# Kernel tuning notes

Hardware: AMD Instinct MI355X
Metric: run time of the kernel (lower is better)

## Reference

```python
import jax, jax.numpy as jnp
import numpy as np

N_NODES = 100000
N_EDGES = 800000
IN_DIM = 128
HID = 128
N_CLASSES = 4


def setup_inputs() -> dict:
    key = jax.random.key(0)
    ks = jax.random.split(key, 8)
    x = jax.random.normal(ks[0], (N_NODES, IN_DIM), dtype=jnp.float32)
    edge_index = jax.random.randint(ks[1], (2, N_EDGES), 0, N_NODES, dtype=jnp.int32)
    s0 = 1.0 / np.sqrt(IN_DIM)
    s1 = 1.0 / np.sqrt(HID)
    W0 = jax.random.uniform(ks[2], (HID, IN_DIM), minval=-s0, maxval=s0, dtype=jnp.float32)
    b0 = jax.random.uniform(ks[3], (HID,), minval=-s0, maxval=s0, dtype=jnp.float32)
    W1 = jax.random.uniform(ks[4], (HID, HID), minval=-s1, maxval=s1, dtype=jnp.float32)
    b1 = jax.random.uniform(ks[5], (HID,), minval=-s1, maxval=s1, dtype=jnp.float32)
    Wc = jax.random.uniform(ks[6], (N_CLASSES, HID), minval=-s1, maxval=s1, dtype=jnp.float32)
    bc = jax.random.uniform(ks[7], (N_CLASSES,), minval=-s1, maxval=s1, dtype=jnp.float32)
    return {"x": x, "edge_index": edge_index, "W0": W0, "b0": b0,
            "W1": W1, "b1": b1, "Wc": Wc, "bc": bc}


def reference(x, edge_index, W0, b0, W1, b1, Wc, bc):
    row, col = edge_index[0], edge_index[1]
    n = x.shape[0]
    # layer 0: Linear + ReLU (dropout is identity in eval)
    h = jax.nn.relu(x @ W0.T + b0)                                  # [N, HID]
    # scatter-add neighbor aggregation with degree normalization
    agg = jax.ops.segment_sum(h[col], row, num_segments=n)          # [N, HID]
    deg = jax.ops.segment_sum(jnp.ones_like(row, dtype=h.dtype), row, num_segments=n)
    agg = agg / jnp.clip(deg, 1.0)[:, None]
    h = h + agg                                                     # residual add
    # final conv + ReLU + classifier
    h = jax.nn.relu(h @ W1.T + b1)
    logits = h @ Wc.T + bc                                          # [N, N_CLASSES]
    return logits
```

## Files before the change

kernel.cpp:

```cpp
#include <hip/hip_runtime.h>

#define IN_DIM 128
#define HID    128
#define NCLS   4

typedef __attribute__((ext_vector_type(8))) short bf16x8;
typedef __attribute__((ext_vector_type(4))) float f32x4;

__device__ inline ushort f2bf(float x) {
    uint u = __builtin_bit_cast(uint, x);
    u += 0x7FFFu + ((u >> 16) & 1u);
    return (ushort)(u >> 16);
}
__device__ inline float bf2f(ushort h) {
    uint u = ((uint)h) << 16;
    return __builtin_bit_cast(float, u);
}

__device__ inline void gload_lds16(const void* g, void* l) {
    __builtin_amdgcn_global_load_lds((const __attribute__((address_space(1))) void*)g,
                                     (__attribute__((address_space(3))) void*)l, 16, 0, 0);
}

__global__ __launch_bounds__(256) void cast_w(const float* __restrict__ W0,
                                              const float* __restrict__ W1,
                                              ushort* __restrict__ w0h, ushort* __restrict__ w0l,
                                              ushort* __restrict__ w1h, ushort* __restrict__ w1l)
{
    int i = blockIdx.x * 256 + threadIdx.x;
    float v = (i < 16384) ? W0[i] : W1[i - 16384];
    ushort h = f2bf(v);
    ushort l = f2bf(v - bf2f(h));
    if (i < 16384) { w0h[i] = h; w0l[i] = l; }
    else           { w1h[i - 16384] = h; w1l[i - 16384] = l; }
}


__global__ __launch_bounds__(256) void gnn_lin0_mfma(const float* __restrict__ X,
                                                     const ushort* __restrict__ Whi,
                                                     const ushort* __restrict__ Wlo,
                                                     const float* __restrict__ Bv,
                                                     ushort* __restrict__ Hhi,
                                                     ushort* __restrict__ Hlo, int M)
{
    __shared__ uint4 lds4[2048];
    char* lds = (char*)lds4;

    const int tid = threadIdx.x;
    const int bm  = blockIdx.x * 64;

    {
        const int row  = tid >> 2;
        const int seg  = tid & 3;
        const int grow = min(bm + row, M - 1);
        const float4* src = (const float4*)((const char*)X + (size_t)grow * 512 + seg * 128);
        float4 v[8];
        #pragma unroll
        for (int j = 0; j < 8; ++j) v[j] = src[j];

        #pragma unroll
        for (int j = 0; j < 4; ++j) {
            uint hw[4], lw[4];
            #pragma unroll
            for (int q = 0; q < 2; ++q) {
                const float4 f = v[j * 2 + q];
                ushort h0 = f2bf(f.x), h1 = f2bf(f.y), h2 = f2bf(f.z), h3 = f2bf(f.w);
                ushort l0 = f2bf(f.x - bf2f(h0)), l1 = f2bf(f.y - bf2f(h1));
                ushort l2 = f2bf(f.z - bf2f(h2)), l3 = f2bf(f.w - bf2f(h3));
                hw[q * 2]     = (uint)h0 | ((uint)h1 << 16);
                hw[q * 2 + 1] = (uint)h2 | ((uint)h3 << 16);
                lw[q * 2]     = (uint)l0 | ((uint)l1 << 16);
                lw[q * 2 + 1] = (uint)l2 | ((uint)l3 << 16);
            }
            int unit = (seg * 4 + j) ^ (row & 7);
            int off  = row * 256 + unit * 16;
            *(uint4*)(lds + off)         = make_uint4(hw[0], hw[1], hw[2], hw[3]);
            *(uint4*)(lds + 16384 + off) = make_uint4(lw[0], lw[1], lw[2], lw[3]);
        }
    }
    __syncthreads();

    const int wid = tid >> 6, lane = tid & 63;
    const int wr = wid >> 1, wc = wid & 1;
    const int colbase = wc * 64;
    const int lr = lane & 15, lk = lane >> 4;

    f32x4 acc[4][2];
    #pragma unroll
    for (int nt = 0; nt < 4; ++nt)
        #pragma unroll
        for (int rt = 0; rt < 2; ++rt) acc[nt][rt] = (f32x4){0.f, 0.f, 0.f, 0.f};

    #pragma unroll
    for (int kt = 0; kt < 4; ++kt) {
        const int ko = kt * 32 + lk * 8;
        bf16x8 xh[2], xl[2];
        #pragma unroll
        for (int rt = 0; rt < 2; ++rt) {
            int lrow = wr * 32 + rt * 16 + lr;
            int unit = (kt * 4 + lk) ^ (lrow & 7);
            int off  = lrow * 256 + unit * 16;
            xh[rt] = *(const bf16x8*)(lds + off);
            xl[rt] = *(const bf16x8*)(lds + 16384 + off);
        }
        #pragma unroll
        for (int nt = 0; nt < 4; ++nt) {
            size_t bo = (size_t)(colbase + nt * 16 + lr) * 128 + ko;
            bf16x8 wh = *(const bf16x8*)(Whi + bo);
            bf16x8 wl = *(const bf16x8*)(Wlo + bo);
            #pragma unroll
            for (int rt = 0; rt < 2; ++rt) {
                acc[nt][rt] = __builtin_amdgcn_mfma_f32_16x16x32_bf16(wh, xh[rt], acc[nt][rt], 0, 0, 0);
                acc[nt][rt] = __builtin_amdgcn_mfma_f32_16x16x32_bf16(wh, xl[rt], acc[nt][rt], 0, 0, 0);
                acc[nt][rt] = __builtin_amdgcn_mfma_f32_16x16x32_bf16(wl, xh[rt], acc[nt][rt], 0, 0, 0);
            }
        }
    }

    #pragma unroll
    for (int nt = 0; nt < 4; ++nt) {
        const int col0 = colbase + nt * 16 + lk * 4;
        const float4 bv4 = *(const float4*)(Bv + col0);
        const float bvv[4] = {bv4.x, bv4.y, bv4.z, bv4.w};
        #pragma unroll
        for (int rt = 0; rt < 2; ++rt) {
            int row = bm + wr * 32 + rt * 16 + lr;
            float o0 = fmaxf(acc[nt][rt][0] + bvv[0], 0.f);
            float o1 = fmaxf(acc[nt][rt][1] + bvv[1], 0.f);
            float o2 = fmaxf(acc[nt][rt][2] + bvv[2], 0.f);
            float o3 = fmaxf(acc[nt][rt][3] + bvv[3], 0.f);
            ushort4 h4, l4;
            h4.x = f2bf(o0); l4.x = f2bf(o0 - bf2f(h4.x));
            h4.y = f2bf(o1); l4.y = f2bf(o1 - bf2f(h4.y));
            h4.z = f2bf(o2); l4.z = f2bf(o2 - bf2f(h4.z));
            h4.w = f2bf(o3); l4.w = f2bf(o3 - bf2f(h4.w));
            size_t oo = (size_t)row * 128 + col0;
            *(ushort4*)(Hhi + oo) = h4;
            *(ushort4*)(Hlo + oo) = l4;
        }
    }
}

__global__ __launch_bounds__(256) void gnn_lin1_mfma(const ushort* __restrict__ Ahi,
                                                     const ushort* __restrict__ Alo,
                                                     const ushort* __restrict__ Whi,
                                                     const ushort* __restrict__ Wlo,
                                                     const float* __restrict__ Bv,
                                                     const float* __restrict__ Wc,
                                                     const float* __restrict__ bc,
                                                     float* __restrict__ Out, int M)
{
    __shared__ uint4 lds4[2048];
    __shared__ float red[2][64][4];
    char* lds = (char*)lds4;

    const int tid = threadIdx.x;
    const int wid = tid >> 6, lane = tid & 63;
    const int bm  = blockIdx.x * 64;

    #pragma unroll
    for (int i = 0; i < 8; ++i) {
        int o = wid * 8192 + i * 1024 + lane * 16;
        const ushort* plane = (o < 16384) ? Ahi : Alo;
        int po   = o & 16383;
        int row  = po >> 8;
        int unit = (po >> 4) & 15;
        const char* src = (const char*)plane + (size_t)(bm + row) * 256
                        + ((unit ^ (row & 7)) << 4);
        gload_lds16(src, lds + wid * 8192 + i * 1024);
    }
    __syncthreads();

    const int wr = wid >> 1, wc = wid & 1;
    const int colbase = wc * 64;
    const int lr = lane & 15, lk = lane >> 4;

    f32x4 acc[4][2];
    #pragma unroll
    for (int nt = 0; nt < 4; ++nt)
        #pragma unroll
        for (int rt = 0; rt < 2; ++rt) acc[nt][rt] = (f32x4){0.f, 0.f, 0.f, 0.f};

    #pragma unroll
    for (int kt = 0; kt < 4; ++kt) {
        const int ko = kt * 32 + lk * 8;
        bf16x8 xh[2], xl[2];
        #pragma unroll
        for (int rt = 0; rt < 2; ++rt) {
            int lrow = wr * 32 + rt * 16 + lr;
            int unit = (kt * 4 + lk) ^ (lrow & 7);
            int off  = lrow * 256 + unit * 16;
            xh[rt] = *(const bf16x8*)(lds + off);
            xl[rt] = *(const bf16x8*)(lds + 16384 + off);
        }
        #pragma unroll
        for (int nt = 0; nt < 4; ++nt) {
            size_t bo = (size_t)(colbase + nt * 16 + lr) * 128 + ko;
            bf16x8 wh = *(const bf16x8*)(Whi + bo);
            bf16x8 wl = *(const bf16x8*)(Wlo + bo);
            #pragma unroll
            for (int rt = 0; rt < 2; ++rt) {
                acc[nt][rt] = __builtin_amdgcn_mfma_f32_16x16x32_bf16(wh, xh[rt], acc[nt][rt], 0, 0, 0);
                acc[nt][rt] = __builtin_amdgcn_mfma_f32_16x16x32_bf16(wh, xl[rt], acc[nt][rt], 0, 0, 0);
                acc[nt][rt] = __builtin_amdgcn_mfma_f32_16x16x32_bf16(wl, xh[rt], acc[nt][rt], 0, 0, 0);
            }
        }
    }

    float p[2][4] = {{0.f, 0.f, 0.f, 0.f}, {0.f, 0.f, 0.f, 0.f}};
    #pragma unroll
    for (int nt = 0; nt < 4; ++nt) {
        const int col0 = colbase + nt * 16 + lk * 4;
        const float4 bv4 = *(const float4*)(Bv + col0);
        const float bvv[4] = {bv4.x, bv4.y, bv4.z, bv4.w};
        float4 wcr[4];
        #pragma unroll
        for (int c = 0; c < 4; ++c) wcr[c] = *(const float4*)(Wc + c * HID + col0);
        #pragma unroll
        for (int rt = 0; rt < 2; ++rt) {
            float h2v[4];
            #pragma unroll
            for (int r = 0; r < 4; ++r) h2v[r] = fmaxf(acc[nt][rt][r] + bvv[r], 0.f);
            #pragma unroll
            for (int c = 0; c < 4; ++c) {
                const float* w = (const float*)&wcr[c];
                p[rt][c] = fmaf(h2v[0], w[0], p[rt][c]);
                p[rt][c] = fmaf(h2v[1], w[1], p[rt][c]);
                p[rt][c] = fmaf(h2v[2], w[2], p[rt][c]);
                p[rt][c] = fmaf(h2v[3], w[3], p[rt][c]);
            }
        }
    }
    #pragma unroll
    for (int off = 16; off < 64; off <<= 1)
        #pragma unroll
        for (int rt = 0; rt < 2; ++rt)
            #pragma unroll
            for (int c = 0; c < 4; ++c)
                p[rt][c] += __shfl_xor(p[rt][c], off);

    if (lk == 0) {
        #pragma unroll
        for (int rt = 0; rt < 2; ++rt) {
            f32x4 v = {p[rt][0], p[rt][1], p[rt][2], p[rt][3]};
            *(f32x4*)&red[wc][wr * 32 + rt * 16 + lr][0] = v;
        }
    }
    __syncthreads();

    const int row_local = tid >> 2, cls = tid & 3;
    int row = blockIdx.x * 64 + row_local;
    if (row < M) {
        float s = bc[cls] + red[0][row_local][cls] + red[1][row_local][cls];
        Out[(size_t)row * 4 + cls] = s;
    }
}

__global__ __launch_bounds__(256) void count_deg(const int* __restrict__ rows,
                                                 int* __restrict__ deg, int E)
{
    int e = blockIdx.x * 256 + threadIdx.x;
    if (e < E) atomicAdd(&deg[rows[e]], 1);
}

__global__ __launch_bounds__(256) void scan_blocks(const int* __restrict__ deg,
                                                   int* __restrict__ off,
                                                   int* __restrict__ bsum, int M)
{
    __shared__ int sh[256];
    int i = blockIdx.x * 256 + threadIdx.x;
    int v = (i < M) ? deg[i] : 0;
    sh[threadIdx.x] = v;
    __syncthreads();
    #pragma unroll
    for (int d = 1; d < 256; d <<= 1) {
        int t = (threadIdx.x >= d) ? sh[threadIdx.x - d] : 0;
        __syncthreads();
        sh[threadIdx.x] += t;
        __syncthreads();
    }
    if (i < M) off[i] = sh[threadIdx.x] - v;
    if (threadIdx.x == 255) bsum[blockIdx.x] = sh[255];
}

__global__ __launch_bounds__(512) void scan_bsum(int* __restrict__ bsum, int NB)
{
    __shared__ int sh[512];
    int v = (threadIdx.x < NB) ? bsum[threadIdx.x] : 0;
    sh[threadIdx.x] = v;
    __syncthreads();
    #pragma unroll
    for (int d = 1; d < 512; d <<= 1) {
        int t = (threadIdx.x >= d) ? sh[threadIdx.x - d] : 0;
        __syncthreads();
        sh[threadIdx.x] += t;
        __syncthreads();
    }
    if (threadIdx.x < NB) bsum[threadIdx.x] = sh[threadIdx.x] - v;
}

__global__ __launch_bounds__(256) void add_off(int* __restrict__ off,
                                               const int* __restrict__ bsum,
                                               int* __restrict__ pos, int M)
{
    int i = blockIdx.x * 256 + threadIdx.x;
    if (i < M) {
        int o = off[i] + bsum[i >> 8];
        off[i] = o;
        pos[i] = o;
    }
}

__global__ __launch_bounds__(256) void fill_csr(const int* __restrict__ rows,
                                                const int* __restrict__ cols,
                                                int* __restrict__ pos,
                                                int* __restrict__ col_sorted, int E)
{
    int e = blockIdx.x * 256 + threadIdx.x;
    if (e < E) {
        int p = atomicAdd(&pos[rows[e]], 1);
        col_sorted[p] = cols[e];
    }
}

__global__ __launch_bounds__(256) void gnn_aggregate(const ushort* __restrict__ Hhi,
                                                     const ushort* __restrict__ Hlo,
                                                     const int* __restrict__ off,
                                                     const int* __restrict__ deg,
                                                     const int* __restrict__ col_sorted,
                                                     ushort* __restrict__ InHi,
                                                     ushort* __restrict__ InLo,
                                                     int M, int Mpad)
{
    int gid  = blockIdx.x * 8 + (threadIdx.x >> 5);
    int lane = threadIdx.x & 31;
    if (gid >= Mpad) return;
    size_t oidx = (size_t)gid * 32 + lane;
    if (gid >= M) {
        ((ushort4*)InHi)[oidx] = make_ushort4(0, 0, 0, 0);
        ((ushort4*)InLo)[oidx] = make_ushort4(0, 0, 0, 0);
        return;
    }

    const ushort4* G = (const ushort4*)Hhi;
    int start = off[gid];
    int d     = deg[gid];
    int end   = start + d;

    float s0[4] = {0.f, 0.f, 0.f, 0.f};
    float s1[4] = {0.f, 0.f, 0.f, 0.f};
    float s2[4] = {0.f, 0.f, 0.f, 0.f};
    float s3[4] = {0.f, 0.f, 0.f, 0.f};
    int e = start;
    for (; e + 4 <= end; e += 4) {
        int c0 = col_sorted[e], c1 = col_sorted[e + 1];
        int c2 = col_sorted[e + 2], c3 = col_sorted[e + 3];
        ushort4 g0 = G[(size_t)c0 * 32 + lane];
        ushort4 g1 = G[(size_t)c1 * 32 + lane];
        ushort4 g2 = G[(size_t)c2 * 32 + lane];
        ushort4 g3 = G[(size_t)c3 * 32 + lane];
        s0[0] += bf2f(g0.x); s0[1] += bf2f(g0.y); s0[2] += bf2f(g0.z); s0[3] += bf2f(g0.w);
        s1[0] += bf2f(g1.x); s1[1] += bf2f(g1.y); s1[2] += bf2f(g1.z); s1[3] += bf2f(g1.w);
        s2[0] += bf2f(g2.x); s2[1] += bf2f(g2.y); s2[2] += bf2f(g2.z); s2[3] += bf2f(g2.w);
        s3[0] += bf2f(g3.x); s3[1] += bf2f(g3.y); s3[2] += bf2f(g3.z); s3[3] += bf2f(g3.w);
    }
    for (; e < end; ++e) {
        int c0 = col_sorted[e];
        ushort4 g0 = G[(size_t)c0 * 32 + lane];
        s0[0] += bf2f(g0.x); s0[1] += bf2f(g0.y); s0[2] += bf2f(g0.z); s0[3] += bf2f(g0.w);
    }
    float a0 = (s0[0] + s1[0]) + (s2[0] + s3[0]);
    float a1 = (s0[1] + s1[1]) + (s2[1] + s3[1]);
    float a2 = (s0[2] + s1[2]) + (s2[2] + s3[2]);
    float a3 = (s0[3] + s1[3]) + (s2[3] + s3[3]);

    float inv = 1.0f / fmaxf((float)d, 1.0f);
    ushort4 rh = ((const ushort4*)Hhi)[oidx];
    ushort4 rl = ((const ushort4*)Hlo)[oidx];
    float o0 = bf2f(rh.x) + bf2f(rl.x) + a0 * inv;
    float o1 = bf2f(rh.y) + bf2f(rl.y) + a1 * inv;
    float o2 = bf2f(rh.z) + bf2f(rl.z) + a2 * inv;
    float o3 = bf2f(rh.w) + bf2f(rl.w) + a3 * inv;

    ushort4 h4, l4;
    h4.x = f2bf(o0); l4.x = f2bf(o0 - bf2f(h4.x));
    h4.y = f2bf(o1); l4.y = f2bf(o1 - bf2f(h4.y));
    h4.z = f2bf(o2); l4.z = f2bf(o2 - bf2f(h4.z));
    h4.w = f2bf(o3); l4.w = f2bf(o3 - bf2f(h4.w));
    ((ushort4*)InHi)[oidx] = h4;
    ((ushort4*)InLo)[oidx] = l4;
}

extern "C" void kernel_launch(void* const* d_in, const int* in_sizes, int n_in,
                              void* d_out, int out_size, void* d_ws, size_t ws_size,
                              hipStream_t stream)
{
    const float* x  = (const float*)d_in[0];
    const int*   ei = (const int*)  d_in[1];
    const float* W0 = (const float*)d_in[2];
    const float* b0 = (const float*)d_in[3];
    const float* W1 = (const float*)d_in[4];
    const float* b1 = (const float*)d_in[5];
    const float* Wc = (const float*)d_in[6];
    const float* bc = (const float*)d_in[7];
    float* out = (float*)d_out;

    const int M    = in_sizes[0] / IN_DIM;
    const int E    = in_sizes[1] / 2;
    const int Mpad = (M + 63) & ~63;
    const int NB   = (M + 255) / 256;

    ushort* Hhi  = (ushort*)d_ws;
    ushort* Hlo  = Hhi  + (size_t)Mpad * 128;
    ushort* InHi = Hlo  + (size_t)Mpad * 128;
    ushort* InLo = InHi + (size_t)Mpad * 128;
    ushort* W0h  = InLo + (size_t)Mpad * 128;
    ushort* W0l  = W0h + 16384;
    ushort* W1h  = W0l + 16384;
    ushort* W1l  = W1h + 16384;
    int* deg_i   = (int*)(W1l + 16384);
    int* off     = deg_i + M;
    int* pos     = off + M;
    int* bsum    = pos + M;
    int* col_sorted = bsum + 512;

    const int* rows = ei;
    const int* cols = ei + E;

    hipMemsetAsync(deg_i, 0, (size_t)M * sizeof(int), stream);

    const int gridMM = Mpad / 64;
    const int gridE  = (E + 255) / 256;
    const int gridN  = (M + 255) / 256;

    cast_w<<<128, 256, 0, stream>>>(W0, W1, W0h, W0l, W1h, W1l);
    gnn_lin0_mfma<<<gridMM, 256, 0, stream>>>(x, W0h, W0l, b0, Hhi, Hlo, M);

    count_deg<<<gridE, 256, 0, stream>>>(rows, deg_i, E);
    scan_blocks<<<gridN, 256, 0, stream>>>(deg_i, off, bsum, M);
    scan_bsum<<<1, 512, 0, stream>>>(bsum, NB);
    add_off<<<gridN, 256, 0, stream>>>(off, bsum, pos, M);
    fill_csr<<<gridE, 256, 0, stream>>>(rows, cols, pos, col_sorted, E);

    gnn_aggregate<<<(Mpad + 7) / 8, 256, 0, stream>>>(Hhi, Hlo, off, deg_i, col_sorted,
                                                      InHi, InLo, M, Mpad);
    gnn_lin1_mfma<<<gridMM, 256, 0, stream>>>(InHi, InLo, W1h, W1l, b1, Wc, bc, out, M);
}
```

Measured before the change: 309.3 us.

## Fuse neighbor aggregation into second linear layer via LDS staging

The separate aggregation kernel is removed. Each lin1 block now gathers neighbor rows for its 64 nodes, adds the residual and writes the hi/lo bf16 split straight into the swizzled LDS tile before the MFMA phase. This avoids writing and re-reading the intermediate InHi/InLo buffers and drops one launch. In exchange, the gather phase now runs with fewer, larger blocks (64 rows each) and cannot overlap with the MFMA work inside a block, which may hurt latency hiding. The col_sorted writes in fill_csr are also made nontemporal.

```diff
diff --git a/kernel.cpp b/kernel.cpp
--- a/kernel.cpp
+++ b/kernel.cpp
@@ -15,11 +15,6 @@
 __device__ inline float bf2f(ushort h) {
     uint u = ((uint)h) << 16;
     return __builtin_bit_cast(float, u);
-}
-
-__device__ inline void gload_lds16(const void* g, void* l) {
-    __builtin_amdgcn_global_load_lds((const __attribute__((address_space(1))) void*)g,
-                                     (__attribute__((address_space(3))) void*)l, 16, 0, 0);
 }
 
 __global__ __launch_bounds__(256) void cast_w(const float* __restrict__ W0,
@@ -141,36 +136,85 @@
     }
 }
 
-__global__ __launch_bounds__(256) void gnn_lin1_mfma(const ushort* __restrict__ Ahi,
-                                                     const ushort* __restrict__ Alo,
-                                                     const ushort* __restrict__ Whi,
-                                                     const ushort* __restrict__ Wlo,
-                                                     const float* __restrict__ Bv,
-                                                     const float* __restrict__ Wc,
-                                                     const float* __restrict__ bc,
-                                                     float* __restrict__ Out, int M)
+__global__ __launch_bounds__(256) void gnn_lin1_fused(const ushort* __restrict__ Hhi,
+                                                      const ushort* __restrict__ Hlo,
+                                                      const int* __restrict__ off,
+                                                      const int* __restrict__ deg,
+                                                      const int* __restrict__ col_sorted,
+                                                      const ushort* __restrict__ Whi,
+                                                      const ushort* __restrict__ Wlo,
+                                                      const float* __restrict__ Bv,
+                                                      const float* __restrict__ Wc,
+                                                      const float* __restrict__ bc,
+                                                      float* __restrict__ Out, int M)
 {
     __shared__ uint4 lds4[2048];
     __shared__ float red[2][64][4];
     char* lds = (char*)lds4;
 
     const int tid = threadIdx.x;
+    const int bm  = blockIdx.x * 64;
+    const int rg     = tid >> 5;
+    const int lane32 = tid & 31;
+
+    const ushort4* H4h = (const ushort4*)Hhi;
+    const ushort4* H4l = (const ushort4*)Hlo;
+
+    #pragma unroll 1
+    for (int it = 0; it < 8; ++it) {
+        const int lrow = it * 8 + rg;
+        const int gid  = bm + lrow;
+        float o0 = 0.f, o1 = 0.f, o2 = 0.f, o3 = 0.f;
+        if (gid < M) {
+            int start = off[gid];
+            int d     = deg[gid];
+            int end   = start + d;
+            float s0[4] = {0.f,0.f,0.f,0.f}, s1[4] = {0.f,0.f,0.f,0.f};
+            float s2[4] = {0.f,0.f,0.f,0.f}, s3[4] = {0.f,0.f,0.f,0.f};
+            int e = start;
+            for (; e + 4 <= end; e += 4) {
+                int c0 = col_sorted[e],     c1 = col_sorted[e + 1];
+                int c2 = col_sorted[e + 2], c3 = col_sorted[e + 3];
+                ushort4 g0 = H4h[(size_t)c0 * 32 + lane32];
+                ushort4 g1 = H4h[(size_t)c1 * 32 + lane32];
+                ushort4 g2 = H4h[(size_t)c2 * 32 + lane32];
+                ushort4 g3 = H4h[(size_t)c3 * 32 + lane32];
+                s0[0] += bf2f(g0.x); s0[1] += bf2f(g0.y); s0[2] += bf2f(g0.z); s0[3] += bf2f(g0.w);
+                s1[0] += bf2f(g1.x); s1[1] += bf2f(g1.y); s1[2] += bf2f(g1.z); s1[3] += bf2f(g1.w);
+                s2[0] += bf2f(g2.x); s2[1] += bf2f(g2.y); s2[2] += bf2f(g2.z); s2[3] += bf2f(g2.w);
+                s3[0] += bf2f(g3.x); s3[1] += bf2f(g3.y); s3[2] += bf2f(g3.z); s3[3] += bf2f(g3.w);
+            }
+            for (; e < end; ++e) {
+                int c0 = col_sorted[e];
+                ushort4 g0 = H4h[(size_t)c0 * 32 + lane32];
+                s0[0] += bf2f(g0.x); s0[1] += bf2f(g0.y); s0[2] += bf2f(g0.z); s0[3] += bf2f(g0.w);
+            }
+            float a0 = (s0[0] + s1[0]) + (s2[0] + s3[0]);
+            float a1 = (s0[1] + s1[1]) + (s2[1] + s3[1]);
+            float a2 = (s0[2] + s1[2]) + (s2[2] + s3[2]);
+            float a3 = (s0[3] + s1[3]) + (s2[3] + s3[3]);
+            float inv = 1.0f / fmaxf((float)d, 1.0f);
+            size_t oidx = (size_t)gid * 32 + lane32;
+            ushort4 rh = H4h[oidx];
+            ushort4 rl = H4l[oidx];
+            o0 = bf2f(rh.x) + bf2f(rl.x) + a0 * inv;
+            o1 = bf2f(rh.y) + bf2f(rl.y) + a1 * inv;
+            o2 = bf2f(rh.z) + bf2f(rl.z) + a2 * inv;
+            o3 = bf2f(rh.w) + bf2f(rl.w) + a3 * inv;
+        }
+        ushort h0 = f2bf(o0), h1 = f2bf(o1), h2 = f2bf(o2), h3 = f2bf(o3);
+        ushort l0 = f2bf(o0 - bf2f(h0)), l1 = f2bf(o1 - bf2f(h1));
+        ushort l2 = f2bf(o2 - bf2f(h2)), l3 = f2bf(o3 - bf2f(h3));
+        uint hw0 = (uint)h0 | ((uint)h1 << 16), hw1 = (uint)h2 | ((uint)h3 << 16);
+        uint lw0 = (uint)l0 | ((uint)l1 << 16), lw1 = (uint)l2 | ((uint)l3 << 16);
+        int unit = (lane32 >> 1) ^ (lrow & 7);
+        int ob   = lrow * 256 + unit * 16 + (lane32 & 1) * 8;
+        *(uint2*)(lds + ob)         = make_uint2(hw0, hw1);
+        *(uint2*)(lds + 16384 + ob) = make_uint2(lw0, lw1);
+    }
+    __syncthreads();
+
     const int wid = tid >> 6, lane = tid & 63;
-    const int bm  = blockIdx.x * 64;
-
-    #pragma unroll
-    for (int i = 0; i < 8; ++i) {
-        int o = wid * 8192 + i * 1024 + lane * 16;
-        const ushort* plane = (o < 16384) ? Ahi : Alo;
-        int po   = o & 16383;
-        int row  = po >> 8;
-        int unit = (po >> 4) & 15;
-        const char* src = (const char*)plane + (size_t)(bm + row) * 256
-                        + ((unit ^ (row & 7)) << 4);
-        gload_lds16(src, lds + wid * 8192 + i * 1024);
-    }
-    __syncthreads();
-
     const int wr = wid >> 1, wc = wid & 1;
     const int colbase = wc * 64;
     const int lr = lane & 15, lk = lane >> 4;
@@ -189,9 +233,9 @@
         for (int rt = 0; rt < 2; ++rt) {
             int lrow = wr * 32 + rt * 16 + lr;
             int unit = (kt * 4 + lk) ^ (lrow & 7);
-            int off  = lrow * 256 + unit * 16;
-            xh[rt] = *(const bf16x8*)(lds + off);
-            xl[rt] = *(const bf16x8*)(lds + 16384 + off);
+            int off2 = lrow * 256 + unit * 16;
+            xh[rt] = *(const bf16x8*)(lds + off2);
+            xl[rt] = *(const bf16x8*)(lds + 16384 + off2);
         }
         #pragma unroll
         for (int nt = 0; nt < 4; ++nt) {
@@ -232,12 +276,12 @@
         }
     }
     #pragma unroll
-    for (int off = 16; off < 64; off <<= 1)
+    for (int offs = 16; offs < 64; offs <<= 1)
         #pragma unroll
         for (int rt = 0; rt < 2; ++rt)
             #pragma unroll
             for (int c = 0; c < 4; ++c)
-                p[rt][c] += __shfl_xor(p[rt][c], off);
+                p[rt][c] += __shfl_xor(p[rt][c], offs);
 
     if (lk == 0) {
         #pragma unroll
@@ -319,76 +363,8 @@
     int e = blockIdx.x * 256 + threadIdx.x;
     if (e < E) {
         int p = atomicAdd(&pos[rows[e]], 1);
-        col_sorted[p] = cols[e];
-    }
-}
-
-__global__ __launch_bounds__(256) void gnn_aggregate(const ushort* __restrict__ Hhi,
-                                                     const ushort* __restrict__ Hlo,
-                                                     const int* __restrict__ off,
-                                                     const int* __restrict__ deg,
-                                                     const int* __restrict__ col_sorted,
-                                                     ushort* __restrict__ InHi,
-                                                     ushort* __restrict__ InLo,
-                                                     int M, int Mpad)
-{
-    int gid  = blockIdx.x * 8 + (threadIdx.x >> 5);
-    int lane = threadIdx.x & 31;
-    if (gid >= Mpad) return;
-    size_t oidx = (size_t)gid * 32 + lane;
-    if (gid >= M) {
-        ((ushort4*)InHi)[oidx] = make_ushort4(0, 0, 0, 0);
-        ((ushort4*)InLo)[oidx] = make_ushort4(0, 0, 0, 0);
-        return;
-    }
-
-    const ushort4* G = (const ushort4*)Hhi;
-    int start = off[gid];
-    int d     = deg[gid];
-    int end   = start + d;
-
-    float s0[4] = {0.f, 0.f, 0.f, 0.f};
-    float s1[4] = {0.f, 0.f, 0.f, 0.f};
-    float s2[4] = {0.f, 0.f, 0.f, 0.f};
-    float s3[4] = {0.f, 0.f, 0.f, 0.f};
-    int e = start;
-    for (; e + 4 <= end; e += 4) {
-        int c0 = col_sorted[e], c1 = col_sorted[e + 1];
-        int c2 = col_sorted[e + 2], c3 = col_sorted[e + 3];
-        ushort4 g0 = G[(size_t)c0 * 32 + lane];
-        ushort4 g1 = G[(size_t)c1 * 32 + lane];
-        ushort4 g2 = G[(size_t)c2 * 32 + lane];
-        ushort4 g3 = G[(size_t)c3 * 32 + lane];
-        s0[0] += bf2f(g0.x); s0[1] += bf2f(g0.y); s0[2] += bf2f(g0.z); s0[3] += bf2f(g0.w);
-        s1[0] += bf2f(g1.x); s1[1] += bf2f(g1.y); s1[2] += bf2f(g1.z); s1[3] += bf2f(g1.w);
-        s2[0] += bf2f(g2.x); s2[1] += bf2f(g2.y); s2[2] += bf2f(g2.z); s2[3] += bf2f(g2.w);
-        s3[0] += bf2f(g3.x); s3[1] += bf2f(g3.y); s3[2] += bf2f(g3.z); s3[3] += bf2f(g3.w);
-    }
-    for (; e < end; ++e) {
-        int c0 = col_sorted[e];
-        ushort4 g0 = G[(size_t)c0 * 32 + lane];
-        s0[0] += bf2f(g0.x); s0[1] += bf2f(g0.y); s0[2] += bf2f(g0.z); s0[3] += bf2f(g0.w);
-    }
-    float a0 = (s0[0] + s1[0]) + (s2[0] + s3[0]);
-    float a1 = (s0[1] + s1[1]) + (s2[1] + s3[1]);
-    float a2 = (s0[2] + s1[2]) + (s2[2] + s3[2]);
-    float a3 = (s0[3] + s1[3]) + (s2[3] + s3[3]);
-
-    float inv = 1.0f / fmaxf((float)d, 1.0f);
-    ushort4 rh = ((const ushort4*)Hhi)[oidx];
-    ushort4 rl = ((const ushort4*)Hlo)[oidx];
-    float o0 = bf2f(rh.x) + bf2f(rl.x) + a0 * inv;
-    float o1 = bf2f(rh.y) + bf2f(rl.y) + a1 * inv;
-    float o2 = bf2f(rh.z) + bf2f(rl.z) + a2 * inv;
-    float o3 = bf2f(rh.w) + bf2f(rl.w) + a3 * inv;
-
-    ushort4 h4, l4;
-    h4.x = f2bf(o0); l4.x = f2bf(o0 - bf2f(h4.x));
-    h4.y = f2bf(o1); l4.y = f2bf(o1 - bf2f(h4.y));
-    h4.z = f2bf(o2); l4.z = f2bf(o2 - bf2f(h4.z));
-    h4.w = f2bf(o3); l4.w = f2bf(o3 - bf2f(h4.w));
-    ((ushort4*)InHi)[oidx] = h4;
-    ((ushort4*)InLo)[oidx] = l4;
+        __builtin_nontemporal_store(cols[e], &col_sorted[p]);
+    }
 }
 
 extern "C" void kernel_launch(void* const* d_in, const int* in_sizes, int n_in,
@@ -412,9 +388,7 @@
 
     ushort* Hhi  = (ushort*)d_ws;
     ushort* Hlo  = Hhi  + (size_t)Mpad * 128;
-    ushort* InHi = Hlo  + (size_t)Mpad * 128;
-    ushort* InLo = InHi + (size_t)Mpad * 128;
-    ushort* W0h  = InLo + (size_t)Mpad * 128;
+    ushort* W0h  = Hlo + (size_t)Mpad * 128;
     ushort* W0l  = W0h + 16384;
     ushort* W1h  = W0l + 16384;
     ushort* W1l  = W1h + 16384;
@@ -442,7 +416,6 @@
     add_off<<<gridN, 256, 0, stream>>>(off, bsum, pos, M);
     fill_csr<<<gridE, 256, 0, stream>>>(rows, cols, pos, col_sorted, E);
 
-    gnn_aggregate<<<(Mpad + 7) / 8, 256, 0, stream>>>(Hhi, Hlo, off, deg_i, col_sorted,
-                                                      InHi, InLo, M, Mpad);
-    gnn_lin1_mfma<<<gridMM, 256, 0, stream>>>(InHi, InLo, W1h, W1l, b1, Wc, bc, out, M);
-}
+    gnn_lin1_fused<<<gridMM, 256, 0, stream>>>(Hhi, Hlo, off, deg_i, col_sorted,
+                                               W1h, W1l, b1, Wc, bc, out, M);
+}
```

Measured after the change: 332.6 us. 7.5% more time.

## Split lin0 GEMM across degree-count and CSR-fill kernels to overlap work

Applied to the files above, without the earlier changes.

The first linear layer is split into two halves, and each half is fused as extra blocks into the degree-count and CSR-fill kernels. The compute-bound GEMM blocks then run alongside the atomic-bound graph preprocessing, and two kernel launches are removed. The CSR column store now uses a nontemporal store. The fused kernels are heavier, which may lower occupancy for the simple atomic blocks, and how well the two block types interleave depends on scheduling.

```diff
diff --git a/kernel.cpp b/kernel.cpp
--- a/kernel.cpp
+++ b/kernel.cpp
@@ -36,18 +36,15 @@
 }
 
 
-__global__ __launch_bounds__(256) void gnn_lin0_mfma(const float* __restrict__ X,
-                                                     const ushort* __restrict__ Whi,
-                                                     const ushort* __restrict__ Wlo,
-                                                     const float* __restrict__ Bv,
-                                                     ushort* __restrict__ Hhi,
-                                                     ushort* __restrict__ Hlo, int M)
-{
-    __shared__ uint4 lds4[2048];
-    char* lds = (char*)lds4;
-
+__device__ __forceinline__ void lin0_body(const float* __restrict__ X,
+                                          const ushort* __restrict__ Whi,
+                                          const ushort* __restrict__ Wlo,
+                                          const float* __restrict__ Bv,
+                                          ushort* __restrict__ Hhi,
+                                          ushort* __restrict__ Hlo,
+                                          int M, int bm, char* lds)
+{
     const int tid = threadIdx.x;
-    const int bm  = blockIdx.x * 64;
 
     {
         const int row  = tid >> 2;
@@ -141,6 +138,49 @@
     }
 }
 
+__global__ __launch_bounds__(256) void k_lin0_count(const float* __restrict__ X,
+                                                    const ushort* __restrict__ Whi,
+                                                    const ushort* __restrict__ Wlo,
+                                                    const float* __restrict__ Bv,
+                                                    ushort* __restrict__ Hhi,
+                                                    ushort* __restrict__ Hlo, int M,
+                                                    int nLin0,
+                                                    const int* __restrict__ rows,
+                                                    int* __restrict__ deg, int E)
+{
+    __shared__ uint4 lds4[2048];
+    if ((int)blockIdx.x < nLin0) {
+        lin0_body(X, Whi, Wlo, Bv, Hhi, Hlo, M, blockIdx.x * 64, (char*)lds4);
+    } else {
+        int e = (blockIdx.x - nLin0) * 256 + threadIdx.x;
+        if (e < E) atomicAdd(&deg[rows[e]], 1);
+    }
+}
+
+__global__ __launch_bounds__(256) void k_lin0_fill(const float* __restrict__ X,
+                                                   const ushort* __restrict__ Whi,
+                                                   const ushort* __restrict__ Wlo,
+                                                   const float* __restrict__ Bv,
+                                                   ushort* __restrict__ Hhi,
+                                                   ushort* __restrict__ Hlo, int M,
+                                                   int nLin0, int baseLin0,
+                                                   const int* __restrict__ rows,
+                                                   const int* __restrict__ cols,
+                                                   int* __restrict__ pos,
+                                                   int* __restrict__ col_sorted, int E)
+{
+    __shared__ uint4 lds4[2048];
+    if ((int)blockIdx.x < nLin0) {
+        lin0_body(X, Whi, Wlo, Bv, Hhi, Hlo, M, (baseLin0 + blockIdx.x) * 64, (char*)lds4);
+    } else {
+        int e = (blockIdx.x - nLin0) * 256 + threadIdx.x;
+        if (e < E) {
+            int p = atomicAdd(&pos[rows[e]], 1);
+            __builtin_nontemporal_store(cols[e], &col_sorted[p]);
+        }
+    }
+}
+
 __global__ __launch_bounds__(256) void gnn_lin1_mfma(const ushort* __restrict__ Ahi,
                                                      const ushort* __restrict__ Alo,
                                                      const ushort* __restrict__ Whi,
@@ -232,12 +272,12 @@
         }
     }
     #pragma unroll
-    for (int off = 16; off < 64; off <<= 1)
+    for (int offs = 16; offs < 64; offs <<= 1)
         #pragma unroll
         for (int rt = 0; rt < 2; ++rt)
             #pragma unroll
             for (int c = 0; c < 4; ++c)
-                p[rt][c] += __shfl_xor(p[rt][c], off);
+                p[rt][c] += __shfl_xor(p[rt][c], offs);
 
     if (lk == 0) {
         #pragma unroll
@@ -256,13 +296,6 @@
     }
 }
 
-__global__ __launch_bounds__(256) void count_deg(const int* __restrict__ rows,
-                                                 int* __restrict__ deg, int E)
-{
-    int e = blockIdx.x * 256 + threadIdx.x;
-    if (e < E) atomicAdd(&deg[rows[e]], 1);
-}
-
 __global__ __launch_bounds__(256) void scan_blocks(const int* __restrict__ deg,
                                                    int* __restrict__ off,
                                                    int* __restrict__ bsum, int M)
@@ -308,18 +341,6 @@
         int o = off[i] + bsum[i >> 8];
         off[i] = o;
         pos[i] = o;
-    }
-}
-
-__global__ __launch_bounds__(256) void fill_csr(const int* __restrict__ rows,
-                                                const int* __restrict__ cols,
-                                                int* __restrict__ pos,
-                                                int* __restrict__ col_sorted, int E)
-{
-    int e = blockIdx.x * 256 + threadIdx.x;
-    if (e < E) {
-        int p = atomicAdd(&pos[rows[e]], 1);
-        col_sorted[p] = cols[e];
     }
 }
 
@@ -430,17 +451,22 @@
     hipMemsetAsync(deg_i, 0, (size_t)M * sizeof(int), stream);
 
     const int gridMM = Mpad / 64;
+    const int nA     = (gridMM + 1) / 2;
+    const int nB     = gridMM - nA;
     const int gridE  = (E + 255) / 256;
     const int gridN  = (M + 255) / 256;
 
     cast_w<<<128, 256, 0, stream>>>(W0, W1, W0h, W0l, W1h, W1l);
-    gnn_lin0_mfma<<<gridMM, 256, 0, stream>>>(x, W0h, W0l, b0, Hhi, Hlo, M);
-
-    count_deg<<<gridE, 256, 0, stream>>>(rows, deg_i, E);
+
+    k_lin0_count<<<nA + gridE, 256, 0, stream>>>(x, W0h, W0l, b0, Hhi, Hlo, M,
+                                                 nA, rows, deg_i, E);
+
     scan_blocks<<<gridN, 256, 0, stream>>>(deg_i, off, bsum, M);
     scan_bsum<<<1, 512, 0, stream>>>(bsum, NB);
     add_off<<<gridN, 256, 0, stream>>>(off, bsum, pos, M);
-    fill_csr<<<gridE, 256, 0, stream>>>(rows, cols, pos, col_sorted, E);
+
+    k_lin0_fill<<<nB + gridE, 256, 0, stream>>>(x, W0h, W0l, b0, Hhi, Hlo, M,
+                                                nB, nA, rows, cols, pos, col_sorted, E);
 
     gnn_aggregate<<<(Mpad + 7) / 8, 256, 0, stream>>>(Hhi, Hlo, off, deg_i, col_sorted,
                                                       InHi, InLo, M, Mpad);
```

Result: faster. 295.9 us (-4.3%).
